# Performance work log

Hardware: AMD Instinct MI355X
Metric: run time of the kernel (lower is better)

## Reference

```python
import jax, jax.numpy as jnp
import numpy as np

B, S, H = 4096, 2048, 64


def setup_inputs() -> dict:
    key = jax.random.key(0)
    ks = jax.random.split(key, 8)
    inp = {
        "returns": jax.random.normal(ks[0], (B, S, 1), dtype=jnp.float32),
        "log_rv": jax.random.normal(ks[1], (B, S, 1), dtype=jnp.float32),
        # scalar GARCH parameters (initialized as in the torch module)
        "omega": jnp.float32(0.01),
        "beta": jnp.float32(0.8),
        "tau1": jnp.float32(0.1),
        "tau2": jnp.float32(0.1),
        "gamma": jnp.float32(0.1),
        "xi": jnp.float32(0.0),
        "phi": jnp.float32(1.0),
        "delta1": jnp.float32(0.1),
        "delta2": jnp.float32(0.1),
        "mu": jnp.float32(0.0),
        # 3 -> H -> H -> 1 MLP weights
        "W1": jax.random.normal(ks[2], (3, H), dtype=jnp.float32) * 0.3,
        "b1": jnp.zeros((H,), dtype=jnp.float32),
        "W2": jax.random.normal(ks[3], (H, H), dtype=jnp.float32) * 0.1,
        "b2": jnp.zeros((H,), dtype=jnp.float32),
        "W3": jax.random.normal(ks[4], (H, 1), dtype=jnp.float32) * 0.1,
        "b3": jnp.zeros((1,), dtype=jnp.float32),
    }
    return inp


def reference(returns, log_rv, omega, beta, tau1, tau2, gamma, xi, phi,
              delta1, delta2, mu, W1, b1, W2, b2, W3, b3):
    # returns, log_rv: [B, S, 1] -> work in time-major [S, B]
    r = jnp.transpose(returns[..., 0])   # [S, B]
    lrv = jnp.transpose(log_rv[..., 0])  # [S, B]

    def mlp(x):  # x: [B, 3]
        h1 = jnp.maximum(x @ W1 + b1, 0.0)
        h2 = jnp.maximum(h1 @ W2 + b2, 0.0)
        return (h2 @ W3 + b3)[..., 0]    # [B]

    def common(log_h, r_t, lrv_t):
        # h_t = exp(log_h); z = (r - mu)/sqrt(h)
        z = (r_t - mu) * jnp.exp(-0.5 * log_h)
        log_x = xi + phi * log_h + delta1 * z + delta2 * (z * z - 1.0)
        u = lrv_t - log_x
        nn_in = jnp.stack([log_h, z, u], axis=-1)  # [B, 3]
        enh_log_h = log_h + 0.01 * mlp(nn_in)
        return enh_log_h, log_x, z, u

    # t = 0: log_h_0 = log(mean(exp(log_rv[:,0:1]))) over a singleton dim = log_rv[:,0]
    lh0, lx0, z0, u0 = common(lrv[0], r[0], lrv[0])

    def step(carry, inp):
        lh_prev, z_prev, lx_prev = carry  # enhanced log_h, z, log_x at t-1
        r_t, lrv_t = inp
        log_h = (omega + beta * lh_prev
                 + tau1 * z_prev + tau2 * (z_prev * z_prev - 1.0)
                 + gamma * lx_prev)
        lh, lx, z, u = common(log_h, r_t, lrv_t)
        return (lh, z, lx), (lh, lx, z, u)

    _, (lh_r, lx_r, z_r, u_r) = jax.lax.scan(step, (lh0, z0, lx0), (r[1:], lrv[1:]))

    def pack(x0, xs):  # [B] + [S-1, B] -> [B, S, 1]
        full = jnp.concatenate([x0[None], xs], axis=0)  # [S, B]
        return jnp.transpose(full)[..., None]

    return (pack(lh0, lh_r), pack(lx0, lx_r), pack(z0, z_r), pack(u0, u_r))
```

## Files before the change

### kernel.cpp

```cpp
#include <hip/hip_runtime.h>

#define BB 4096
#define SS 2048
#define TCH 128
#define WRM 64
#define NCH (SS / TCH)

typedef __attribute__((ext_vector_type(8))) short short8;
typedef __attribute__((ext_vector_type(16))) float f32x16;

union frag8 { unsigned u[4]; short8 s; };

__device__ __forceinline__ unsigned pk_bf16(float a, float b) {
    unsigned ua = __float_as_uint(a);
    unsigned ub = __float_as_uint(b);
    ua = (ua + 0x7FFFu + ((ua >> 16) & 1u)) >> 16;
    ub = (ub + 0x7FFFu + ((ub >> 16) & 1u)) >> 16;
    return ua | (ub << 16);
}

__device__ __forceinline__ unsigned cvt_pk(float a, float b) {
    unsigned r;
    asm("v_cvt_pk_bf16_f32 %0, %1, %2" : "=v"(r) : "v"(a), "v"(b));
    return r;
}

__device__ __forceinline__ int rho_k(int c, int k) {
    return 16 * c + (k & 3) + 8 * ((k >> 2) & 1) + 4 * (k >> 3);
}

__global__ __launch_bounds__(64, 2) void garch_pinn_kernel(
    const float* __restrict__ returns_p, const float* __restrict__ log_rv_p,
    const float* __restrict__ p_omega, const float* __restrict__ p_beta,
    const float* __restrict__ p_tau1, const float* __restrict__ p_tau2,
    const float* __restrict__ p_gamma, const float* __restrict__ p_xi,
    const float* __restrict__ p_phi, const float* __restrict__ p_delta1,
    const float* __restrict__ p_delta2, const float* __restrict__ p_mu,
    const float* __restrict__ W1, const float* __restrict__ b1,
    const float* __restrict__ W2, const float* __restrict__ b2,
    const float* __restrict__ W3, const float* __restrict__ b3,
    float* __restrict__ out)
{
    const int lane = threadIdx.x;
    const int s    = lane & 31;
    const int g    = lane >> 5;
    const int bid  = blockIdx.x;
    const int sg   = bid & (BB / 32 - 1);
    const int c    = bid >> 7;
    const int base = sg * 32;

    const int tbeg   = (c == 0) ? 0 : (c * TCH - WRM);
    const int warm   = c * TCH - tbeg;
    const int nsteps = (c + 1) * TCH - tbeg;

    __shared__ float2 rv[32][34];
    __shared__ float4 obuf[32][17];

    const float omega  = p_omega[0],  beta   = p_beta[0];
    const float tau1   = p_tau1[0],   tau2   = p_tau2[0];
    const float gamma_ = p_gamma[0],  xi     = p_xi[0];
    const float phi    = p_phi[0];
    const float delta1 = p_delta1[0], delta2 = p_delta2[0];
    const float mu     = p_mu[0],     b3s    = b3[0];

    const float ky = 0.01f * beta;
    const float qc = omega - tau2 + ky * b3s;
    const float lc = xi - delta2;

    frag8 A1[2];
    #pragma unroll
    for (int t = 0; t < 2; ++t) {
        const int j = 32 * t + s;
        float v[8];
        #pragma unroll
        for (int kk = 0; kk < 8; ++kk) {
            const int k = 8 * g + kk;
            float val = 0.f;
            if (k == 0)      val = W1[j];
            else if (k == 1) val = W1[64 + j];
            else if (k == 2) val = -W1[128 + j];
            else if (k == 3) val = W1[128 + j];
            else if (k == 4) val = b1[j];
            v[kk] = val;
        }
        #pragma unroll
        for (int p = 0; p < 4; ++p) A1[t].u[p] = pk_bf16(v[2 * p], v[2 * p + 1]);
    }

    frag8 A2[2][4];
    #pragma unroll
    for (int t2 = 0; t2 < 2; ++t2) {
        const int j = 32 * t2 + s;
        #pragma unroll
        for (int cc = 0; cc < 4; ++cc) {
            float v[8];
            #pragma unroll
            for (int kk = 0; kk < 8; ++kk)
                v[kk] = W2[rho_k(cc, 8 * g + kk) * 64 + j];
            #pragma unroll
            for (int p = 0; p < 4; ++p) A2[t2][cc].u[p] = pk_bf16(v[2 * p], v[2 * p + 1]);
        }
    }

    frag8 A3[4];
    #pragma unroll
    for (int cc = 0; cc < 4; ++cc) {
        float v[8];
        #pragma unroll
        for (int kk = 0; kk < 8; ++kk)
            v[kk] = (s == 0) ? W3[rho_k(cc, 8 * g + kk)] : 0.f;
        #pragma unroll
        for (int p = 0; p < 4; ++p) A3[cc].u[p] = pk_bf16(v[2 * p], v[2 * p + 1]);
    }

    f32x16 b2c0, b2c1;
    #pragma unroll
    for (int reg = 0; reg < 16; ++reg) {
        const int row = (reg & 3) + 8 * (reg >> 2) + 4 * g;
        b2c0[reg] = b2[row];
        b2c1[reg] = b2[32 + row];
    }

    f32x16 zero16;
    #pragma unroll
    for (int p = 0; p < 16; ++p) zero16[p] = 0.f;

    float* const out_lh = out;
    float* const out_lx = out + (size_t)BB * SS;
    float* const out_z  = out + (size_t)2 * BB * SS;
    float* const out_u  = out + (size_t)3 * BB * SS;

    float q_st = log_rv_p[(size_t)(base + s) * SS + tbeg];
    float y_st = 0.f;

    float rpre[16], vpre[16];
    #pragma unroll
    for (int q = 0; q < 16; ++q) {
        const size_t col = (size_t)(base + 2 * q + g) * SS + tbeg + (lane & 31);
        rpre[q] = returns_p[col];
        vpre[q] = log_rv_p[col];
    }

    for (int t0 = 0; t0 < nsteps; t0 += 32) {
        #pragma unroll
        for (int q = 0; q < 16; ++q) {
            float2 w; w.x = rpre[q]; w.y = vpre[q];
            rv[2 * q + g][lane & 31] = w;
        }
        __builtin_amdgcn_wave_barrier();
        if (t0 + 32 < nsteps) {
            #pragma unroll
            for (int q = 0; q < 16; ++q) {
                const size_t col = (size_t)(base + 2 * q + g) * SS
                                 + tbeg + t0 + 32 + (lane & 31);
                rpre[q] = returns_p[col];
                vpre[q] = log_rv_p[col];
            }
        }

        const bool emit = (t0 >= warm);

        #pragma unroll 1
        for (int half = 0; half < 2; ++half) {
            #pragma unroll 4
            for (int pp = 0; pp < 8; ++pp) {
                const float4 xq = *reinterpret_cast<const float4*>(
                                      &rv[s][half * 16 + 2 * pp]);
                #pragma unroll
                for (int sub = 0; sub < 2; ++sub) {
                    const int   i2  = 2 * pp + sub;
                    const float r_t = sub ? xq.z : xq.x;
                    const float v_t = sub ? xq.w : xq.y;

                    const float log_h = fmaf(ky, y_st, q_st);
                    const float lb = fmaf(0.01f, b3s, log_h);
                    const float rm = r_t - mu;
                    const float ea = log_h * -0.72134752044448f;
                    float ex; asm("v_exp_f32 %0, %1" : "=v"(ex) : "v"(ea));
                    const float z  = rm * ex;
                    const float zz = z * z;
                    const float lx = fmaf(delta2, zz, fmaf(delta1, z, fmaf(phi, log_h, lc)));
                    const float u  = v_t - lx;
                    q_st = fmaf(beta, log_h,
                            fmaf(tau1, z, fmaf(tau2, zz, fmaf(gamma_, lx, qc))));

                    frag8 Bx;
                    const unsigned w0 = cvt_pk(log_h, z);
                    const unsigned w1 = cvt_pk(lx, v_t);
                    Bx.u[0] = g ? 0u : w0;
                    Bx.u[1] = g ? 0u : w1;
                    Bx.u[2] = g ? 0u : 0x3f80u;
                    Bx.u[3] = 0u;

                    __builtin_amdgcn_s_setprio(1);
                    f32x16 c1a = __builtin_amdgcn_mfma_f32_32x32x16_bf16(A1[0].s, Bx.s, zero16, 0, 0, 0);
                    f32x16 c1b = __builtin_amdgcn_mfma_f32_32x32x16_bf16(A1[1].s, Bx.s, zero16, 0, 0, 0);

                    frag8 Bh[4];
                    #pragma unroll
                    for (int p = 0; p < 4; ++p) {
                        Bh[0].u[p] = cvt_pk(fmaxf(c1a[2 * p],     0.f), fmaxf(c1a[2 * p + 1],     0.f));
                        Bh[1].u[p] = cvt_pk(fmaxf(c1a[8 + 2 * p], 0.f), fmaxf(c1a[8 + 2 * p + 1], 0.f));
                        Bh[2].u[p] = cvt_pk(fmaxf(c1b[2 * p],     0.f), fmaxf(c1b[2 * p + 1],     0.f));
                        Bh[3].u[p] = cvt_pk(fmaxf(c1b[8 + 2 * p], 0.f), fmaxf(c1b[8 + 2 * p + 1], 0.f));
                    }

                    f32x16 c2a = b2c0, c2b = b2c1;
                    #pragma unroll
                    for (int cc = 0; cc < 4; ++cc) {
                        c2a = __builtin_amdgcn_mfma_f32_32x32x16_bf16(A2[0][cc].s, Bh[cc].s, c2a, 0, 0, 0);
                        c2b = __builtin_amdgcn_mfma_f32_32x32x16_bf16(A2[1][cc].s, Bh[cc].s, c2b, 0, 0, 0);
                    }

                    frag8 Bh2[4];
                    #pragma unroll
                    for (int p = 0; p < 4; ++p) {
                        Bh2[0].u[p] = cvt_pk(fmaxf(c2a[2 * p],     0.f), fmaxf(c2a[2 * p + 1],     0.f));
                        Bh2[1].u[p] = cvt_pk(fmaxf(c2a[8 + 2 * p], 0.f), fmaxf(c2a[8 + 2 * p + 1], 0.f));
                        Bh2[2].u[p] = cvt_pk(fmaxf(c2b[2 * p],     0.f), fmaxf(c2b[2 * p + 1],     0.f));
                        Bh2[3].u[p] = cvt_pk(fmaxf(c2b[8 + 2 * p], 0.f), fmaxf(c2b[8 + 2 * p + 1], 0.f));
                    }

                    f32x16 c3a = __builtin_amdgcn_mfma_f32_32x32x16_bf16(A3[0].s, Bh2[0].s, zero16, 0, 0, 0);
                    c3a = __builtin_amdgcn_mfma_f32_32x32x16_bf16(A3[1].s, Bh2[1].s, c3a, 0, 0, 0);
                    f32x16 c3b = __builtin_amdgcn_mfma_f32_32x32x16_bf16(A3[2].s, Bh2[2].s, zero16, 0, 0, 0);
                    c3b = __builtin_amdgcn_mfma_f32_32x32x16_bf16(A3[3].s, Bh2[3].s, c3b, 0, 0, 0);
                    __builtin_amdgcn_s_setprio(0);
                    const float y0 = c3a[0] + c3b[0];

                    float a = y0, yb = y0;
                    asm("v_permlane32_swap_b32 %0, %1" : "+v"(a), "+v"(yb));
                    const float ytot = yb;

                    const float enh = fmaf(0.01f, ytot, lb);
                    y_st = ytot;

                    if (lane < 32) {
                        float4 o; o.x = enh; o.y = lx; o.z = z; o.w = u;
                        obuf[s][i2] = o;
                    }
                }
            }

            __builtin_amdgcn_wave_barrier();
            if (emit) {
                const int w  = lane & 15;
                const int qh = lane >> 4;
                const int tg = tbeg + t0 + half * 16;
                #pragma unroll
                for (int grp = 0; grp < 8; ++grp) {
                    const int q = 4 * grp + qh;
                    const float4 o = obuf[q][w];
                    const size_t col = (size_t)(base + q) * SS + tg + w;
                    out_lh[col] = o.x;
                    out_lx[col] = o.y;
                    out_z [col] = o.z;
                    out_u [col] = o.w;
                }
            }
            __builtin_amdgcn_wave_barrier();
        }
    }
}

extern "C" void kernel_launch(void* const* d_in, const int* in_sizes, int n_in,
                              void* d_out, int out_size, void* d_ws, size_t ws_size,
                              hipStream_t stream) {
    (void)in_sizes; (void)n_in; (void)out_size; (void)d_ws; (void)ws_size;
    hipLaunchKernelGGL(garch_pinn_kernel, dim3((BB / 32) * NCH), dim3(64), 0, stream,
                       (const float*)d_in[0], (const float*)d_in[1],
                       (const float*)d_in[2], (const float*)d_in[3],
                       (const float*)d_in[4], (const float*)d_in[5],
                       (const float*)d_in[6], (const float*)d_in[7],
                       (const float*)d_in[8], (const float*)d_in[9],
                       (const float*)d_in[10], (const float*)d_in[11],
                       (const float*)d_in[12], (const float*)d_in[13],
                       (const float*)d_in[14], (const float*)d_in[15],
                       (const float*)d_in[16], (const float*)d_in[17],
                       (float*)d_out);
}
```

Before: 182.4 us.

## Replace final MLP layer MFMAs with VALU dot, shrink time chunks for more blocks

The third MLP layer (64->1) is now computed as a per-lane FMA dot product over the MFMA accumulator rows, with a permlane32 swap to sum the two half-waves, instead of four MFMAs plus the bf16 repacking. This shortens the serial per-timestep dependency chain and keeps W3 in fp32. The time chunk length is halved, which doubles the number of blocks for parallelism but makes the 64-step warm-up a larger fraction of the work. Launch bounds are raised to three blocks per SIMD and the inner unroll is reduced to ease register pressure. Bx is no longer zeroed for the upper half-wave, which may change the MFMA input layout.

```diff
diff --git a/kernel.cpp b/kernel.cpp
--- a/kernel.cpp
+++ b/kernel.cpp
@@ -2,7 +2,7 @@
 
 #define BB 4096
 #define SS 2048
-#define TCH 128
+#define TCH 64
 #define WRM 64
 #define NCH (SS / TCH)
 
@@ -29,7 +29,7 @@
     return 16 * c + (k & 3) + 8 * ((k >> 2) & 1) + 4 * (k >> 3);
 }
 
-__global__ __launch_bounds__(64, 2) void garch_pinn_kernel(
+__global__ __launch_bounds__(64, 3) void garch_pinn_kernel(
     const float* __restrict__ returns_p, const float* __restrict__ log_rv_p,
     const float* __restrict__ p_omega, const float* __restrict__ p_beta,
     const float* __restrict__ p_tau1, const float* __restrict__ p_tau2,
@@ -63,9 +63,10 @@
     const float delta1 = p_delta1[0], delta2 = p_delta2[0];
     const float mu     = p_mu[0],     b3s    = b3[0];
 
-    const float ky = 0.01f * beta;
-    const float qc = omega - tau2 + ky * b3s;
-    const float lc = xi - delta2;
+    const float ky  = 0.01f * beta;
+    const float qc  = omega - tau2 + ky * b3s;
+    const float lc  = xi - delta2;
+    const float cb3 = 0.01f * b3s;
 
     frag8 A1[2];
     #pragma unroll
@@ -102,23 +103,15 @@
         }
     }
 
-    frag8 A3[4];
-    #pragma unroll
-    for (int cc = 0; cc < 4; ++cc) {
-        float v[8];
-        #pragma unroll
-        for (int kk = 0; kk < 8; ++kk)
-            v[kk] = (s == 0) ? W3[rho_k(cc, 8 * g + kk)] : 0.f;
-        #pragma unroll
-        for (int p = 0; p < 4; ++p) A3[cc].u[p] = pk_bf16(v[2 * p], v[2 * p + 1]);
-    }
-
     f32x16 b2c0, b2c1;
+    float w3a[16], w3b[16];
     #pragma unroll
     for (int reg = 0; reg < 16; ++reg) {
         const int row = (reg & 3) + 8 * (reg >> 2) + 4 * g;
         b2c0[reg] = b2[row];
         b2c1[reg] = b2[32 + row];
+        w3a[reg]  = W3[row];
+        w3b[reg]  = W3[32 + row];
     }
 
     f32x16 zero16;
@@ -162,7 +155,7 @@
 
         #pragma unroll 1
         for (int half = 0; half < 2; ++half) {
-            #pragma unroll 4
+            #pragma unroll 2
             for (int pp = 0; pp < 8; ++pp) {
                 const float4 xq = *reinterpret_cast<const float4*>(
                                       &rv[s][half * 16 + 2 * pp]);
@@ -173,7 +166,7 @@
                     const float v_t = sub ? xq.w : xq.y;
 
                     const float log_h = fmaf(ky, y_st, q_st);
-                    const float lb = fmaf(0.01f, b3s, log_h);
+                    const float lb = log_h + cb3;
                     const float rm = r_t - mu;
                     const float ea = log_h * -0.72134752044448f;
                     float ex; asm("v_exp_f32 %0, %1" : "=v"(ex) : "v"(ea));
@@ -185,11 +178,9 @@
                             fmaf(tau1, z, fmaf(tau2, zz, fmaf(gamma_, lx, qc))));
 
                     frag8 Bx;
-                    const unsigned w0 = cvt_pk(log_h, z);
-                    const unsigned w1 = cvt_pk(lx, v_t);
-                    Bx.u[0] = g ? 0u : w0;
-                    Bx.u[1] = g ? 0u : w1;
-                    Bx.u[2] = g ? 0u : 0x3f80u;
+                    Bx.u[0] = cvt_pk(log_h, z);
+                    Bx.u[1] = cvt_pk(lx, v_t);
+                    Bx.u[2] = 0x3f80u;
                     Bx.u[3] = 0u;
 
                     __builtin_amdgcn_s_setprio(1);
@@ -211,26 +202,21 @@
                         c2a = __builtin_amdgcn_mfma_f32_32x32x16_bf16(A2[0][cc].s, Bh[cc].s, c2a, 0, 0, 0);
                         c2b = __builtin_amdgcn_mfma_f32_32x32x16_bf16(A2[1][cc].s, Bh[cc].s, c2b, 0, 0, 0);
                     }
-
-                    frag8 Bh2[4];
+                    __builtin_amdgcn_s_setprio(0);
+
+                    float ya = 0.f, yb2 = 0.f, yc = 0.f, yd = 0.f;
                     #pragma unroll
-                    for (int p = 0; p < 4; ++p) {
-                        Bh2[0].u[p] = cvt_pk(fmaxf(c2a[2 * p],     0.f), fmaxf(c2a[2 * p + 1],     0.f));
-                        Bh2[1].u[p] = cvt_pk(fmaxf(c2a[8 + 2 * p], 0.f), fmaxf(c2a[8 + 2 * p + 1], 0.f));
-                        Bh2[2].u[p] = cvt_pk(fmaxf(c2b[2 * p],     0.f), fmaxf(c2b[2 * p + 1],     0.f));
-                        Bh2[3].u[p] = cvt_pk(fmaxf(c2b[8 + 2 * p], 0.f), fmaxf(c2b[8 + 2 * p + 1], 0.f));
-                    }
-
-                    f32x16 c3a = __builtin_amdgcn_mfma_f32_32x32x16_bf16(A3[0].s, Bh2[0].s, zero16, 0, 0, 0);
-                    c3a = __builtin_amdgcn_mfma_f32_32x32x16_bf16(A3[1].s, Bh2[1].s, c3a, 0, 0, 0);
-                    f32x16 c3b = __builtin_amdgcn_mfma_f32_32x32x16_bf16(A3[2].s, Bh2[2].s, zero16, 0, 0, 0);
-                    c3b = __builtin_amdgcn_mfma_f32_32x32x16_bf16(A3[3].s, Bh2[3].s, c3b, 0, 0, 0);
-                    __builtin_amdgcn_s_setprio(0);
-                    const float y0 = c3a[0] + c3b[0];
-
-                    float a = y0, yb = y0;
-                    asm("v_permlane32_swap_b32 %0, %1" : "+v"(a), "+v"(yb));
-                    const float ytot = yb;
+                    for (int reg = 0; reg < 16; reg += 2) {
+                        ya  = fmaf(fmaxf(c2a[reg],     0.f), w3a[reg],     ya);
+                        yb2 = fmaf(fmaxf(c2a[reg + 1], 0.f), w3a[reg + 1], yb2);
+                        yc  = fmaf(fmaxf(c2b[reg],     0.f), w3b[reg],     yc);
+                        yd  = fmaf(fmaxf(c2b[reg + 1], 0.f), w3b[reg + 1], yd);
+                    }
+                    float y = (ya + yb2) + (yc + yd);
+
+                    float a = y, bsw = y;
+                    asm("v_permlane32_swap_b32 %0, %1" : "+v"(a), "+v"(bsw));
+                    const float ytot = y + bsw;
 
                     const float enh = fmaf(0.01f, ytot, lb);
                     y_st = ytot;
```

After: 429.3 us. 135% more time.
